# Kernel tuning notes

Hardware: AMD Instinct MI355X
Metric: run time of the kernel (lower is better)

Reference implementation:

```python
import jax, jax.numpy as jnp
import numpy as np

B = 2048
MAX_ATOMS = 32
ELEM = 83
LATENT = 64
LATTICE = 9


def _lin(k, fin, fout):
    k1, k2 = jax.random.split(k)
    s = 1.0 / np.sqrt(fin)
    return (jax.random.uniform(k1, (fin, fout), jnp.float32, -s, s),
            jax.random.uniform(k2, (fout,), jnp.float32, -s, s))


def setup_inputs() -> dict:
    key = jax.random.key(0)
    ks = jax.random.split(key, 32)
    inp = {}
    inp['elements'] = jax.random.randint(ks[0], (B, MAX_ATOMS), 0, ELEM)
    inp['coords'] = jax.random.uniform(ks[1], (B, MAX_ATOMS, 3), jnp.float32)
    inp['lattice'] = jax.random.normal(ks[2], (B, LATTICE), jnp.float32)
    inp['composition'] = jax.random.uniform(ks[3], (B, ELEM), jnp.float32)
    inp['eps'] = jax.random.normal(ks[4], (B, LATENT), jnp.float32)
    inp['emb_table'] = jax.random.normal(ks[5], (ELEM, 16), jnp.float32)
    inp['enc_w1'], inp['enc_b1'] = _lin(ks[6], 19, 256)
    inp['enc_w2'], inp['enc_b2'] = _lin(ks[7], 256, 128)
    inp['enc_w3'], inp['enc_b3'] = _lin(ks[8], 128, 128)
    inp['lat_w1'], inp['lat_b1'] = _lin(ks[9], LATTICE, 64)
    inp['lat_w2'], inp['lat_b2'] = _lin(ks[10], 64, 64)
    inp['mu_w'], inp['mu_b'] = _lin(ks[11], 192, LATENT)
    inp['lv_w'], inp['lv_b'] = _lin(ks[12], 192, LATENT)
    inp['dec_w1'], inp['dec_b1'] = _lin(ks[13], LATENT + ELEM, 512)
    s1 = 1.0 / np.sqrt(64 * 27)
    inp['ct1_w'] = jax.random.uniform(ks[14], (32, 64, 3, 3, 3), jnp.float32, -s1, s1)
    inp['ct1_b'] = jax.random.uniform(ks[15], (32,), jnp.float32, -s1, s1)
    s2 = 1.0 / np.sqrt(32 * 27)
    inp['ct2_w'] = jax.random.uniform(ks[16], (16, 32, 3, 3, 3), jnp.float32, -s2, s2)
    inp['ct2_b'] = jax.random.uniform(ks[17], (16,), jnp.float32, -s2, s2)
    inp['dec_w2'], inp['dec_b2'] = _lin(ks[18], 16 * 8 * 8 * 8, MAX_ATOMS * (ELEM + 3))
    inp['dl_w1'], inp['dl_b1'] = _lin(ks[19], LATENT, 64)
    inp['dl_w2'], inp['dl_b2'] = _lin(ks[20], 64, LATTICE)
    inp['gat1_w'], _ = _lin(ks[21], 19, 3 * 64)
    inp['gat1_b'] = jnp.zeros((3 * 64,), jnp.float32)
    inp['gat1_as'] = jax.random.normal(ks[22], (3, 64), jnp.float32) * 0.1
    inp['gat1_ad'] = jax.random.normal(ks[23], (3, 64), jnp.float32) * 0.1
    inp['gat2_w'], _ = _lin(ks[24], 192, 3)
    inp['gat2_b'] = jnp.zeros((3,), jnp.float32)
    inp['gat2_as'] = jax.random.normal(ks[25], (1, 3), jnp.float32) * 0.1
    inp['gat2_ad'] = jax.random.normal(ks[26], (1, 3), jnp.float32) * 0.1
    return inp


def _convT(x, w, b):
    # ConvTranspose3d(k=3, stride=2, pad=1, output_pad=1) == input-dilated conv
    y = jax.lax.conv_general_dilated(
        x, w, window_strides=(1, 1, 1),
        padding=((1, 2), (1, 2), (1, 2)), lhs_dilation=(2, 2, 2),
        dimension_numbers=('NCDHW', 'OIDHW', 'NCDHW'))
    return y + b[None, :, None, None, None]


def _gat(x, W, a_src, a_dst, bias, heads, out_ch, concat):
    # Dense (fully-connected per-sample graph) GATConv, eval mode (dropout off).
    Bn, N, F = x.shape
    h = jnp.einsum('bnf,fhc->bnhc', x, W.reshape(F, heads, out_ch))  # [B,N,H,C]
    s = jnp.einsum('bnhc,hc->bnh', h, a_src)  # source scores
    d = jnp.einsum('bnhc,hc->bnh', h, a_dst)  # target scores
    # e[b,i,j,h] for edge j->i (self-loops included in the full mesh)
    e = jax.nn.leaky_relu(d[:, :, None, :] + s[:, None, :, :], 0.2)
    a = jax.nn.softmax(e, axis=2)  # softmax over sources j per target i
    o = jnp.einsum('bijh,bjhc->bihc', a, h)
    if concat:
        return o.reshape(Bn, N, heads * out_ch) + bias
    return o.mean(axis=2) + bias


def reference(elements, coords, lattice, composition, eps, emb_table,
              enc_w1, enc_b1, enc_w2, enc_b2, enc_w3, enc_b3,
              lat_w1, lat_b1, lat_w2, lat_b2, mu_w, mu_b, lv_w, lv_b,
              dec_w1, dec_b1, ct1_w, ct1_b, ct2_w, ct2_b, dec_w2, dec_b2,
              dl_w1, dl_b1, dl_w2, dl_b2,
              gat1_w, gat1_b, gat1_as, gat1_ad,
              gat2_w, gat2_b, gat2_as, gat2_ad):
    Bn = coords.shape[0]
    # ---- encode ----
    af = jnp.concatenate([emb_table[elements], coords], axis=-1)  # [B,32,19]
    h = jax.nn.relu(af @ enc_w1 + enc_b1)
    h = jax.nn.relu(h @ enc_w2 + enc_b2)
    h = h @ enc_w3 + enc_b3
    g = h.mean(axis=1)  # [B,128]
    l = jax.nn.relu(lattice @ lat_w1 + lat_b1) @ lat_w2 + lat_b2
    comb = jnp.concatenate([g, l], axis=1)
    mu = comb @ mu_w + mu_b
    logvar = comb @ lv_w + lv_b
    z = mu + eps * jnp.exp(0.5 * logvar)
    # ---- decode ----
    d = jnp.concatenate([z, composition], axis=1) @ dec_w1 + dec_b1
    d = d.reshape(Bn, 64, 2, 2, 2)
    d = jax.nn.relu(_convT(d, ct1_w, ct1_b))   # [B,32,4,4,4]
    d = jax.nn.relu(_convT(d, ct2_w, ct2_b))   # [B,16,8,8,8]
    raw = (d.reshape(Bn, -1) @ dec_w2 + dec_b2).reshape(Bn, MAX_ATOMS, ELEM + 3)
    logits = raw[..., :ELEM]
    init_coords = jax.nn.sigmoid(raw[..., ELEM:])
    node = jnp.concatenate([emb_table[jnp.argmax(logits, axis=-1)], init_coords], axis=-1)  # [B,32,19]
    x = jax.nn.elu(_gat(node, gat1_w, gat1_as, gat1_ad, gat1_b, 3, 64, True))
    adj = jnp.tanh(_gat(x, gat2_w, gat2_as, gat2_ad, gat2_b, 1, 3, False)) * 0.1
    coords_out = jnp.mod(init_coords + adj, 1.0)
    recon = jnp.concatenate([logits, coords_out], axis=-1)  # [B,32,86]
    recon_lattice = jax.nn.relu(z @ dl_w1 + dl_b1) @ dl_w2 + dl_b2
    return (mu, logvar, recon, recon_lattice)
```

## Files before the change

kernel.cpp:

```cpp
#include <hip/hip_runtime.h>
#include <hip/hip_bf16.h>

typedef __hip_bfloat16 bf16;
typedef __attribute__((ext_vector_type(8))) __bf16 bf16x8;
typedef __attribute__((ext_vector_type(4))) float f32x4;

__device__ __forceinline__ float b2f(bf16 v){ return __bfloat162float(v); }
__device__ __forceinline__ bf16  f2b(float v){ return __float2bfloat16(v); }

template<typename T> __device__ __forceinline__ float ldf(const T* p, size_t i);
template<> __device__ __forceinline__ float ldf<float>(const float* p, size_t i){ return p[i]; }
template<> __device__ __forceinline__ float ldf<bf16 >(const bf16*  p, size_t i){ return b2f(p[i]); }

template<typename T> __device__ __forceinline__ void stf(T* p, size_t i, float v);
template<> __device__ __forceinline__ void stf<float>(float* p, size_t i, float v){ p[i] = v; }
template<> __device__ __forceinline__ void stf<bf16 >(bf16*  p, size_t i, float v){ p[i] = f2b(v); }

#define NATM 32
#define RECON_OFF 262144
#define RL_OFF    5898240

__device__ __forceinline__ void glds16(const bf16* g, bf16* l){
    __builtin_amdgcn_global_load_lds(
        (const __attribute__((address_space(1))) unsigned int*)g,
        (__attribute__((address_space(3))) unsigned int*)l,
        16, 0, 0);
}

__global__ __launch_bounds__(64) void k_detect(const void* emb, int* flag)
{
    __shared__ int cnt[64];
    const int t = threadIdx.x;
    const unsigned short* p = (const unsigned short*)emb;
    int c = 0;
    for (int i = t; i < 256; i += 64){
        int e = (p[i] >> 7) & 0xFF;
        c += (e >= 110 && e <= 132) ? 1 : 0;
    }
    cnt[t] = c;
    __syncthreads();
    if (t == 0){
        int s = 0;
        for (int i = 0; i < 64; i++) s += cnt[i];
        *flag = (s >= 200) ? 1 : 0;
    }
}

template<typename T>
__device__ __forceinline__ void prepEnc_impl(
    const T* w1, const T* b1, const T* w2, const T* b2,
    bf16* W1t, bf16* W2t, float* ebias)
{
    const int gt = blockIdx.x*256 + threadIdx.x;
    const int gs = gridDim.x*256;
    for (int e = gt; e < 8192; e += gs){
        int n = e >> 5, k = e & 31;
        W1t[e] = (k < 19) ? f2b(ldf(w1, (size_t)k*256 + n)) : f2b(0.f);
    }
    for (int e = gt; e < 32768; e += gs){
        int n = e >> 8, k = e & 255;
        W2t[e] = f2b(ldf(w2, (size_t)k*128 + n));
    }
    for (int i = gt; i < 384; i += gs)
        ebias[i] = (i < 256) ? ldf(b1, i) : ldf(b2, i-256);
}

__global__ __launch_bounds__(256) void k_prepEnc(
    const int* flag, const void* w1, const void* b1, const void* w2, const void* b2,
    bf16* W1t, bf16* W2t, float* ebias)
{
    if (*flag) prepEnc_impl<bf16>((const bf16*)w1,(const bf16*)b1,(const bf16*)w2,(const bf16*)b2, W1t, W2t, ebias);
    else       prepEnc_impl<float>((const float*)w1,(const float*)b1,(const float*)w2,(const float*)b2, W1t, W2t, ebias);
}

template<typename T>
__device__ __forceinline__ void buildA_impl(
    const int* elements, const T* coords, const T* emb, bf16* Abuf)
{
    const int r = blockIdx.x*256 + threadIdx.x;
    const int el = elements[r];
    bf16 row[32];
    #pragma unroll
    for (int f=0; f<16; f++) row[f] = f2b(ldf(emb, (size_t)el*16 + f));
    #pragma unroll
    for (int c=0; c<3; c++) row[16+c] = f2b(ldf(coords, (size_t)r*3 + c));
    #pragma unroll
    for (int f=19; f<32; f++) row[f] = f2b(0.f);
    *(int4*)(&Abuf[(size_t)r*32])      = *(int4*)(&row[0]);
    *(int4*)(&Abuf[(size_t)r*32 + 8])  = *(int4*)(&row[8]);
    *(int4*)(&Abuf[(size_t)r*32 + 16]) = *(int4*)(&row[16]);
    *(int4*)(&Abuf[(size_t)r*32 + 24]) = *(int4*)(&row[24]);
}

__global__ __launch_bounds__(256) void k_buildA(
    const int* flag, const int* elements, const void* coords, const void* emb, bf16* Abuf)
{
    if (*flag) buildA_impl<bf16>(elements,(const bf16*)coords,(const bf16*)emb, Abuf);
    else       buildA_impl<float>(elements,(const float*)coords,(const float*)emb, Abuf);
}

template<typename T>
__device__ __forceinline__ void pool_impl(
    const float* h2, const T* w3, const T* b3, float* gbuf)
{
    __shared__ float hsum[128];
    const int b = blockIdx.x, t = threadIdx.x;
    float s = 0.f;
    for (int n=0; n<32; n++) s += h2[(size_t)(b*32+n)*128 + t];
    hsum[t] = s;
    __syncthreads();
    float a = 0.f;
    for (int k=0; k<128; k++) a += hsum[k]*ldf(w3, (size_t)k*128 + t);
    gbuf[b*128+t] = a*(1.f/32.f) + ldf(b3, t);
}

__global__ __launch_bounds__(128) void k_pool(
    const int* flag, const float* h2, const void* w3, const void* b3, float* gbuf)
{
    if (*flag) pool_impl<bf16>(h2, (const bf16*)w3, (const bf16*)b3, gbuf);
    else       pool_impl<float>(h2, (const float*)w3, (const float*)b3, gbuf);
}

template<typename T>
__device__ __forceinline__ void enc_impl(
    const int* elements, const T* coords, const T* emb,
    const T* w1, const T* b1, const T* w2, const T* b2c,
    const T* w3, const T* b3, float* gbuf, char* smem)
{
    float (*af)[19]   = (float(*)[19])(smem);
    float (*h1)[256]  = (float(*)[256])(smem + 2432);
    float (*h2s)[128] = (float(*)[128])(smem + 35200);
    float* hsum       = (float*)(smem + 51584);
    const int b = blockIdx.x, t = threadIdx.x;

    for (int idx = t; idx < NATM*19; idx += 256){
        int n = idx/19, f = idx - n*19;
        af[n][f] = (f < 16) ? ldf(emb, (size_t)elements[b*NATM+n]*16 + f)
                            : ldf(coords, (size_t)(b*NATM+n)*3 + (f-16));
    }
    __syncthreads();
    {
        float wc[19];
        #pragma unroll
        for (int f=0; f<19; f++) wc[f] = ldf(w1, f*256 + t);
        float bb = ldf(b1, t);
        for (int n=0; n<NATM; n++){
            float a = bb;
            #pragma unroll
            for (int f=0; f<19; f++) a += af[n][f]*wc[f];
            h1[n][t] = fmaxf(a, 0.f);
        }
    }
    __syncthreads();
    {
        const int j = t & 127, half = t >> 7;
        float bb = ldf(b2c, j);
        float acc[16];
        #pragma unroll
        for (int n=0;n<16;n++) acc[n] = bb;
        for (int k=0;k<256;k+=4){
            float wa = ldf(w2, (k+0)*128+j);
            float wb = ldf(w2, (k+1)*128+j);
            float wcv= ldf(w2, (k+2)*128+j);
            float wd = ldf(w2, (k+3)*128+j);
            #pragma unroll
            for (int n=0;n<16;n++){
                float4 hv = *(const float4*)(&h1[half*16+n][k]);
                acc[n] += hv.x*wa + hv.y*wb + hv.z*wcv + hv.w*wd;
            }
        }
        #pragma unroll
        for (int n=0;n<16;n++) h2s[half*16+n][j] = fmaxf(acc[n], 0.f);
    }
    __syncthreads();
    if (t < 128){
        float s = 0.f;
        for (int n=0;n<NATM;n++) s += h2s[n][t];
        hsum[t] = s;
    }
    __syncthreads();
    if (t < 128){
        float a = 0.f;
        for (int k=0;k<128;k++) a += hsum[k]*ldf(w3, k*128+t);
        gbuf[b*128+t] = a*(1.f/32.f) + ldf(b3, t);
    }
}

__global__ __launch_bounds__(256) void k_encoder(
    const int* flag, const int* elements, const void* coords, const void* emb,
    const void* w1, const void* b1, const void* w2, const void* b2,
    const void* w3, const void* b3, float* gbuf)
{
    __shared__ __align__(16) char smem[52096];
    if (*flag) enc_impl<bf16>(elements,(const bf16*)coords,(const bf16*)emb,
        (const bf16*)w1,(const bf16*)b1,(const bf16*)w2,(const bf16*)b2,
        (const bf16*)w3,(const bf16*)b3, gbuf, smem);
    else       enc_impl<float>(elements,(const float*)coords,(const float*)emb,
        (const float*)w1,(const float*)b1,(const float*)w2,(const float*)b2,
        (const float*)w3,(const float*)b3, gbuf, smem);
}

template<typename T>
__device__ __forceinline__ void lat_impl(
    const T* lattice, const T* eps, const T* comp,
    const T* lw1, const T* lb1, const T* lw2, const T* lb2,
    const T* muw, const T* mub, const T* lvw, const T* lvb,
    const T* dw1, const T* db1, const T* dw2, const T* db2,
    const float* gbuf, float* zbuf, bf16* zc, void* d_out, char* smem)
{
    float* comb = (float*)(smem);
    float* lat  = (float*)(smem + 768);
    float* l1   = (float*)(smem + 832);
    float* zz   = (float*)(smem + 1088);
    float* r1   = (float*)(smem + 1344);
    T* out_mu = (T*)d_out;
    T* out_lv = out_mu + 131072;
    T* out_rl = out_mu + RL_OFF;
    const int b = blockIdx.x, t = threadIdx.x;
    comb[t]    = gbuf[b*128 + t];
    comb[64+t] = gbuf[b*128 + 64 + t];
    if (t < 9) lat[t] = ldf(lattice, b*9 + t);
    __syncthreads();
    {
        float a = ldf(lb1, t);
        #pragma unroll
        for (int f=0; f<9; f++) a += lat[f]*ldf(lw1, f*64+t);
        l1[t] = fmaxf(a, 0.f);
    }
    __syncthreads();
    {
        float a = ldf(lb2, t);
        for (int k=0;k<64;k++) a += l1[k]*ldf(lw2, k*64+t);
        comb[128+t] = a;
    }
    __syncthreads();
    float mu = ldf(mub, t), lv = ldf(lvb, t);
    for (int k=0;k<192;k++){
        float c = comb[k];
        mu += c*ldf(muw, k*64+t);
        lv += c*ldf(lvw, k*64+t);
    }
    float z = mu + ldf(eps, b*64+t)*expf(0.5f*lv);
    stf(out_mu, (size_t)b*64+t, mu);
    stf(out_lv, (size_t)b*64+t, lv);
    zbuf[b*64+t] = z;
    zz[t] = z;
    __syncthreads();
    if (zc){
        for (int i=t; i<160; i+=64){
            float v = (i<64) ? zz[i] : ((i<147) ? ldf(comp, b*83 + (i-64)) : 0.f);
            zc[(size_t)b*160 + i] = f2b(v);
        }
    }
    {
        float a = ldf(db1, t);
        for (int k=0;k<64;k++) a += zz[k]*ldf(dw1, k*64+t);
        r1[t] = fmaxf(a, 0.f);
    }
    __syncthreads();
    if (t < 9){
        float a = ldf(db2, t);
        for (int k=0;k<64;k++) a += r1[k]*ldf(dw2, k*9+t);
        stf(out_rl, (size_t)b*9+t, a);
    }
}

__global__ __launch_bounds__(64) void k_latent(
    const int* flag, const void* lattice, const void* eps, const void* comp,
    const void* lw1, const void* lb1, const void* lw2, const void* lb2,
    const void* muw, const void* mub, const void* lvw, const void* lvb,
    const void* dw1, const void* db1, const void* dw2, const void* db2,
    const float* gbuf, float* zbuf, bf16* zc, void* d_out)
{
    __shared__ __align__(16) char smem[1600];
    if (*flag) lat_impl<bf16>((const bf16*)lattice,(const bf16*)eps,(const bf16*)comp,
        (const bf16*)lw1,(const bf16*)lb1,(const bf16*)lw2,(const bf16*)lb2,
        (const bf16*)muw,(const bf16*)mub,(const bf16*)lvw,(const bf16*)lvb,
        (const bf16*)dw1,(const bf16*)db1,(const bf16*)dw2,(const bf16*)db2,
        gbuf, zbuf, zc, d_out, smem);
    else       lat_impl<float>((const float*)lattice,(const float*)eps,(const float*)comp,
        (const float*)lw1,(const float*)lb1,(const float*)lw2,(const float*)lb2,
        (const float*)muw,(const float*)mub,(const float*)lvw,(const float*)lvb,
        (const float*)dw1,(const float*)db1,(const float*)dw2,(const float*)db2,
        gbuf, zbuf, zc, d_out, smem);
}

template<typename T>
__device__ __forceinline__ void prep_impl(
    const T* db1, const T* c1b, const T* c2b, const T* db2, const T* dw1,
    float* biasf, bf16* BtW1)
{
    const int gt = blockIdx.x*256 + threadIdx.x;
    const int gs = gridDim.x*256;
    for (int i = gt; i < 3376; i += gs){
        float v;
        if (i < 512)      v = ldf(db1, i);
        else if (i < 544) v = ldf(c1b, i-512);
        else if (i < 560) v = ldf(c2b, i-544);
        else              v = (i-560 < 2752) ? ldf(db2, i-560) : 0.f;
        biasf[i] = v;
    }
    for (int e = gt; e < 512*160; e += gs){
        int n = e/160, k = e - n*160;
        BtW1[e] = f2b((k < 147) ? ldf(dw1, (size_t)k*512 + n) : 0.f);
    }
}

__global__ __launch_bounds__(256) void k_prep(
    const int* flag, const void* db1, const void* c1b, const void* c2b,
    const void* db2, const void* dw1, float* biasf, bf16* BtW1)
{
    if (*flag) prep_impl<bf16>((const bf16*)db1,(const bf16*)c1b,(const bf16*)c2b,
        (const bf16*)db2,(const bf16*)dw1, biasf, BtW1);
    else       prep_impl<float>((const float*)db1,(const float*)c1b,(const float*)c2b,
        (const float*)db2,(const float*)dw1, biasf, BtW1);
}

template<typename T>
__device__ __forceinline__ void expWc1_impl(const T* w, bf16* Wc1T)
{
    const int t = threadIdx.x;
    const int n = blockIdx.x*4 + (t >> 6);
    const int k0 = (t & 63) << 3;
    const int o = n >> 6, spo = n & 63;
    const int zd = spo >> 4, zh = (spo >> 2) & 3, zw = spo & 3;
    bf16 v8[8];
    #pragma unroll
    for (int j = 0; j < 8; j++){
        int k = k0 + j;
        int i = k >> 3, sp = k & 7;
        int td = sp >> 2, th = (sp >> 1) & 1, tw = sp & 1;
        int kd = 2*td + 1 - zd, kh = 2*th + 1 - zh, kw = 2*tw + 1 - zw;
        float v = 0.f;
        if (kd >= 0 && kd < 3 && kh >= 0 && kh < 3 && kw >= 0 && kw < 3)
            v = ldf(w, (size_t)(o*64 + i)*27 + kd*9 + kh*3 + kw);
        v8[j] = f2b(v);
    }
    *(int4*)(&Wc1T[(size_t)n*512 + k0]) = *(int4*)v8;
}

__global__ __launch_bounds__(256) void k_expWc1(const int* flag, const void* w, bf16* Wc1T)
{
    if (*flag) expWc1_impl<bf16>((const bf16*)w, Wc1T);
    else       expWc1_impl<float>((const float*)w, Wc1T);
}

template<typename T>
__device__ __forceinline__ void expWc2_impl(const T* w, bf16* Wc2T)
{
    const int n = blockIdx.x;
    const int k0 = threadIdx.x << 3;
    const int o = n >> 9, spo = n & 511;
    const int zd = spo >> 6, zh = (spo >> 3) & 7, zw = spo & 7;
    bf16 v8[8];
    #pragma unroll
    for (int j = 0; j < 8; j++){
        int k = k0 + j;
        int i = k >> 6, sp = k & 63;
        int td = sp >> 4, th = (sp >> 2) & 3, tw = sp & 3;
        int kd = 2*td + 1 - zd, kh = 2*th + 1 - zh, kw = 2*tw + 1 - zw;
        float v = 0.f;
        if (kd >= 0 && kd < 3 && kh >= 0 && kh < 3 && kw >= 0 && kw < 3)
            v = ldf(w, (size_t)(o*32 + i)*27 + kd*9 + kh*3 + kw);
        v8[j] = f2b(v);
    }
    *(int4*)(&Wc2T[(size_t)n*2048 + k0]) = *(int4*)v8;
}

__global__ __launch_bounds__(256) void k_expWc2(const int* flag, const void* w, bf16* Wc2T)
{
    if (*flag) expWc2_impl<bf16>((const bf16*)w, Wc2T);
    else       expWc2_impl<float>((const float*)w, Wc2T);
}

template<typename T>
__device__ __forceinline__ void transW_impl(const T* B, bf16* Bt)
{
    __shared__ bf16 tile[64][65];
    const int kb = blockIdx.x << 6;
    const int nb = blockIdx.y << 6;
    const int t = threadIdx.x;
    for (int idx=t; idx<4096; idx+=256){
        int k = idx>>6, n = idx&63;
        int col = nb + n;
        tile[k][n] = (col < 2752) ? f2b(ldf(B, (size_t)(kb+k)*2752 + col)) : f2b(0.f);
    }
    __syncthreads();
    for (int idx=t; idx<4096; idx+=256){
        int n = idx>>6, k = idx&63;
        Bt[(size_t)(nb+n)*8192 + kb + k] = tile[k][n];
    }
}

__global__ __launch_bounds__(256) void k_transW(const int* flag, const void* B, bf16* Bt)
{
    if (*flag) transW_impl<bf16>((const bf16*)B, Bt);
    else       transW_impl<float>((const float*)B, Bt);
}

struct GemmAcc { f32x4 a[4][4]; };

__device__ __forceinline__ void gemm128_core(
    const bf16* __restrict__ A, const bf16* __restrict__ Bt, int K,
    int bm, int bn, bf16* As, bf16* Bs, GemmAcc& G)
{
    const int t = threadIdx.x;
    const int w = t >> 6, lane = t & 63;
    const int wm = w >> 1, wn = w & 1;
    const int ml = lane & 15, mq = lane >> 4;
    const int lrow = lane >> 2;
    const int gchunk = (lane & 3) ^ ((lane >> 3) & 3);
    const int rchunk = (mq ^ ((ml >> 1) & 3)) << 3;

    const size_t arow = (size_t)(bm + w*32 + lrow);
    const size_t brow = (size_t)(bn + w*32 + lrow);

    for (int kt = 0; kt < K; kt += 32){
        __syncthreads();
        #pragma unroll
        for (int c = 0; c < 2; c++){
            glds16(A  + (arow + c*16)*K + kt + gchunk*8, &As[(w*32 + c*16)*32]);
            glds16(Bt + (brow + c*16)*K + kt + gchunk*8, &Bs[(w*32 + c*16)*32]);
        }
        __syncthreads();
        bf16x8 af[4], bfr[4];
        #pragma unroll
        for (int i=0;i<4;i++) af[i]  = *(const bf16x8*)(&As[(wm*64 + i*16 + ml)*32 + rchunk]);
        #pragma unroll
        for (int j=0;j<4;j++) bfr[j] = *(const bf16x8*)(&Bs[(wn*64 + j*16 + ml)*32 + rchunk]);
        #pragma unroll
        for (int i=0;i<4;i++)
            #pragma unroll
            for (int j=0;j<4;j++)
                G.a[i][j] = __builtin_amdgcn_mfma_f32_16x16x32_bf16(af[i], bfr[j], G.a[i][j], 0,0,0);
    }
}

template<typename OutT, int ACT>
__global__ __launch_bounds__(256) void k_gemm128(
    const bf16* __restrict__ A, const bf16* __restrict__ Bt, int K,
    const float* __restrict__ biasf, int bshift,
    OutT* __restrict__ C, int ldc)
{
    __shared__ __align__(16) bf16 As[128*32];
    __shared__ __align__(16) bf16 Bs[128*32];
    const int t = threadIdx.x;
    const int bm = blockIdx.x << 7, bn = blockIdx.y << 7;
    const int w = t >> 6, lane = t & 63;
    const int wm = w >> 1, wn = w & 1;
    const int ml = lane & 15, mq = lane >> 4;
    GemmAcc G;
    #pragma unroll
    for (int i=0;i<4;i++)
        #pragma unroll
        for (int j=0;j<4;j++) G.a[i][j] = (f32x4){0.f,0.f,0.f,0.f};
    gemm128_core(A, Bt, K, bm, bn, As, Bs, G);
    #pragma unroll
    for (int j=0;j<4;j++){
        const int col = bn + wn*64 + (j<<4) + ml;
        const float bv = biasf[col >> bshift];
        #pragma unroll
        for (int i=0;i<4;i++){
            #pragma unroll
            for (int r=0;r<4;r++){
                const int row = bm + wm*64 + (i<<4) + (mq<<2) + r;
                float v = G.a[i][j][r] + bv;
                if (ACT == 1) v = fmaxf(v, 0.f);
                stf(C, (size_t)row*ldc + col, v);
            }
        }
    }
}

__global__ __launch_bounds__(256) void k_gemm_recon64(
    const int* __restrict__ flag,
    const bf16* __restrict__ A, const bf16* __restrict__ Bt,
    const float* __restrict__ biasf, void* __restrict__ d_out)
{
    __shared__ __align__(16) bf16 As[64*32];
    __shared__ __align__(16) bf16 Bs[128*32];
    const int K = 8192;
    const int t = threadIdx.x;
    const int bm = blockIdx.x << 6, bn = blockIdx.y << 7;
    const int w = t >> 6, lane = t & 63;
    const int wm = w >> 1, wn = w & 1;
    const int ml = lane & 15, mq = lane >> 4;
    const int lrow = lane >> 2;
    const int gchunk = (lane & 3) ^ ((lane >> 3) & 3);
    const int rchunk = (mq ^ ((ml >> 1) & 3)) << 3;

    f32x4 acc[2][4];
    #pragma unroll
    for (int i=0;i<2;i++)
        #pragma unroll
        for (int j=0;j<4;j++) acc[i][j] = (f32x4){0.f,0.f,0.f,0.f};

    const size_t arow = (size_t)(bm + w*16 + lrow);
    const size_t brow = (size_t)(bn + w*32 + lrow);

    for (int kt = 0; kt < K; kt += 32){
        __syncthreads();
        glds16(A + arow*K + kt + gchunk*8, &As[(w*16)*32]);
        #pragma unroll
        for (int c = 0; c < 2; c++)
            glds16(Bt + (brow + c*16)*K + kt + gchunk*8, &Bs[(w*32 + c*16)*32]);
        __syncthreads();
        bf16x8 af[2], bfr[4];
        #pragma unroll
        for (int i=0;i<2;i++) af[i]  = *(const bf16x8*)(&As[(wm*32 + i*16 + ml)*32 + rchunk]);
        #pragma unroll
        for (int j=0;j<4;j++) bfr[j] = *(const bf16x8*)(&Bs[(wn*64 + j*16 + ml)*32 + rchunk]);
        #pragma unroll
        for (int i=0;i<2;i++)
            #pragma unroll
            for (int j=0;j<4;j++)
                acc[i][j] = __builtin_amdgcn_mfma_f32_16x16x32_bf16(af[i], bfr[j], acc[i][j], 0,0,0);
    }
    const int fl = *flag;
    #pragma unroll
    for (int j=0;j<4;j++){
        const int col = bn + wn*64 + (j<<4) + ml;
        if (col >= 2752) continue;
        const int f = col % 86;
        const float bv = biasf[560 + col];
        #pragma unroll
        for (int i=0;i<2;i++){
            #pragma unroll
            for (int r=0;r<4;r++){
                const int row = bm + wm*32 + (i<<4) + (mq<<2) + r;
                float v = acc[i][j][r] + bv;
                if (f >= 83) v = 1.f/(1.f + expf(-v));
                if (fl) stf((bf16*)d_out + RECON_OFF, (size_t)row*2752 + col, v);
                else    stf((float*)d_out + RECON_OFF, (size_t)row*2752 + col, v);
            }
        }
    }
}

template<typename T>
__device__ __forceinline__ void conv_impl(
    const float* zbuf, const T* comp,
    const T* dw1, const T* db1, const T* c1w, const T* c1b,
    const T* c2w, const T* c2b, bf16* Amat, char* smem)
{
    float* zc        = (float*)(smem);
    float (*d0s)[8]  = (float(*)[8])(smem + 640);
    float (*c1s)[64] = (float(*)[64])(smem + 2688);
    bf16* w2s        = (bf16*)(smem + 10880);
    const int b = blockIdx.x, t = threadIdx.x;
    for (int i=t; i<16*32*27; i+=256) w2s[i] = f2b(ldf(c2w, i));
    if (t < 147) zc[t] = (t < 64) ? zbuf[b*64+t] : ldf(comp, b*83 + (t-64));
    __syncthreads();
    #pragma unroll
    for (int jj=0; jj<2; jj++){
        int j = t + (jj<<8);
        float a = ldf(db1, j);
        for (int k=0;k<147;k++) a += zc[k]*ldf(dw1, k*512+j);
        d0s[j>>3][j&7] = a;
    }
    __syncthreads();
    {
        const int o = t>>3;
        const float bias = ldf(c1b, o);
        const T* wb = c1w + o*64*27;
        for (int u=0; u<8; u++){
            int sp = (t&7) + (u<<3);
            int zd = sp>>4, zh = (sp>>2)&3, zw = sp&3;
            float acc = bias;
            for (int kd=0;kd<3;kd++){
                int qd = zd+kd-1; if (qd<0 || (qd&1) || qd>=4) continue; int td=qd>>1;
                for (int kh=0;kh<3;kh++){
                    int qh = zh+kh-1; if (qh<0 || (qh&1) || qh>=4) continue; int th=qh>>1;
                    for (int kw=0;kw<3;kw++){
                        int qw = zw+kw-1; if (qw<0 || (qw&1) || qw>=4) continue; int tw=qw>>1;
                        const int koff = kd*9+kh*3+kw;
                        const int spi = td*4+th*2+tw;
                        float s = 0.f;
                        #pragma unroll 8
                        for (int i=0;i<64;i++) s += ldf(wb, i*27+koff)*d0s[i][spi];
                        acc += s;
                    }
                }
            }
            c1s[o][sp] = fmaxf(acc, 0.f);
        }
    }
    __syncthreads();
    {
        const int o = t>>4;
        const float bias = ldf(c2b, o);
        for (int u=0; u<32; u++){
            int sp = (t&15) + (u<<4);
            int zd = sp>>6, zh=(sp>>3)&7, zw=sp&7;
            float acc = bias;
            for (int kd=0;kd<3;kd++){
                int qd = zd+kd-1; if (qd<0 || (qd&1) || qd>=8) continue; int td=qd>>1;
                for (int kh=0;kh<3;kh++){
                    int qh = zh+kh-1; if (qh<0 || (qh&1) || qh>=8) continue; int th=qh>>1;
                    for (int kw=0;kw<3;kw++){
                        int qw = zw+kw-1; if (qw<0 || (qw&1) || qw>=8) continue; int tw=qw>>1;
                        const int koff = kd*9+kh*3+kw;
                        const int spi = td*16+th*4+tw;
                        const int wbase = (o*32)*27 + koff;
                        float s = 0.f;
                        #pragma unroll 8
                        for (int i=0;i<32;i++) s += b2f(w2s[wbase + i*27])*c1s[i][spi];
                        acc += s;
                    }
                }
            }
            Amat[(size_t)b*8192 + o*512 + sp] = f2b(fmaxf(acc, 0.f));
        }
    }
}

__global__ __launch_bounds__(256) void k_conv(
    const int* flag, const float* zbuf, const void* comp,
    const void* dw1, const void* db1, const void* c1w, const void* c1b,
    const void* c2w, const void* c2b, bf16* Amat)
{
    __shared__ __align__(16) char smem[38528];
    if (*flag) conv_impl<bf16>(zbuf,(const bf16*)comp,(const bf16*)dw1,(const bf16*)db1,
        (const bf16*)c1w,(const bf16*)c1b,(const bf16*)c2w,(const bf16*)c2b, Amat, smem);
    else       conv_impl<float>(zbuf,(const float*)comp,(const float*)dw1,(const float*)db1,
        (const float*)c1w,(const float*)c1b,(const float*)c2w,(const float*)c2b, Amat, smem);
}

template<typename T> struct BStage;
template<> struct BStage<bf16>{
    static __device__ __forceinline__ void go(const bf16* p, bf16* v8){
        union{ int4 q; bf16 e[8]; } u; u.q = *(const int4*)p;
        #pragma unroll
        for (int j=0;j<8;j++) v8[j] = u.e[j];
    }
};
template<> struct BStage<float>{
    static __device__ __forceinline__ void go(const float* p, bf16* v8){
        float4 a = *(const float4*)p, b = *(const float4*)(p+4);
        v8[0]=f2b(a.x); v8[1]=f2b(a.y); v8[2]=f2b(a.z); v8[3]=f2b(a.w);
        v8[4]=f2b(b.x); v8[5]=f2b(b.y); v8[6]=f2b(b.z); v8[7]=f2b(b.w);
    }
};

__device__ __forceinline__ bf16x8 readBfrag(const bf16 (*Bs)[42], int n, int k0){
    union { bf16x8 v; unsigned int u[4]; } r;
    const unsigned int* p = (const unsigned int*)(&Bs[n][k0]);
    r.u[0]=p[0]; r.u[1]=p[1]; r.u[2]=p[2]; r.u[3]=p[3];
    return r.v;
}

template<typename T>
__device__ __forceinline__ void gemm_impl(
    const bf16* A, const T* B, const T* bias, void* d_out, char* smem)
{
    bf16 (*As)[40] = (bf16(*)[40])(smem);
    bf16 (*Bs)[42] = (bf16(*)[42])(smem + 10240);
    T* out_recon = (T*)d_out + RECON_OFF;
    const int t = threadIdx.x;
    const int bm = blockIdx.x << 7;
    const int bn = blockIdx.y << 6;
    const int w = t >> 6, lane = t & 63;
    const int ml = lane & 15, mq = lane >> 4;
    f32x4 acc[2][4];
    #pragma unroll
    for (int i=0;i<2;i++)
        #pragma unroll
        for (int j=0;j<4;j++) acc[i][j] = (f32x4){0.f,0.f,0.f,0.f};

    const int sm = t >> 2;
    const int sk = (t & 3) << 3;
    const int kk = t >> 3;
    const int nn = (t & 7) << 3;

    for (int kt = 0; kt < 8192; kt += 32){
        __syncthreads();
        {
            int4 v0 = *(const int4*)(A + (size_t)(bm + sm     )*8192 + kt + sk);
            int4 v1 = *(const int4*)(A + (size_t)(bm + sm + 64)*8192 + kt + sk);
            *(int4*)(&As[sm][sk])    = v0;
            *(int4*)(&As[sm+64][sk]) = v1;
            bf16 bv[8];
            BStage<T>::go(B + (size_t)(kt + kk)*2752 + bn + nn, bv);
            #pragma unroll
            for (int j=0;j<8;j++) Bs[nn+j][kk] = bv[j];
        }
        __syncthreads();
        bf16x8 a0 = *(const bf16x8*)(&As[(w<<5) + ml     ][mq<<3]);
        bf16x8 a1 = *(const bf16x8*)(&As[(w<<5) + 16 + ml][mq<<3]);
        bf16x8 b0 = readBfrag(Bs, ml,      mq<<3);
        bf16x8 b1 = readBfrag(Bs, 16 + ml, mq<<3);
        bf16x8 b2 = readBfrag(Bs, 32 + ml, mq<<3);
        bf16x8 b3 = readBfrag(Bs, 48 + ml, mq<<3);
        acc[0][0] = __builtin_amdgcn_mfma_f32_16x16x32_bf16(a0,b0,acc[0][0],0,0,0);
        acc[0][1] = __builtin_amdgcn_mfma_f32_16x16x32_bf16(a0,b1,acc[0][1],0,0,0);
        acc[0][2] = __builtin_amdgcn_mfma_f32_16x16x32_bf16(a0,b2,acc[0][2],0,0,0);
        acc[0][3] = __builtin_amdgcn_mfma_f32_16x16x32_bf16(a0,b3,acc[0][3],0,0,0);
        acc[1][0] = __builtin_amdgcn_mfma_f32_16x16x32_bf16(a1,b0,acc[1][0],0,0,0);
        acc[1][1] = __builtin_amdgcn_mfma_f32_16x16x32_bf16(a1,b1,acc[1][1],0,0,0);
        acc[1][2] = __builtin_amdgcn_mfma_f32_16x16x32_bf16(a1,b2,acc[1][2],0,0,0);
        acc[1][3] = __builtin_amdgcn_mfma_f32_16x16x32_bf16(a1,b3,acc[1][3],0,0,0);
    }
    #pragma unroll
    for (int nt=0; nt<4; nt++){
        const int col = bn + (nt<<4) + ml;
        const int atom = col / 86;
        const int f = col - atom*86;
        const float bv = ldf(bias, col);
        #pragma unroll
        for (int mt=0; mt<2; mt++){
            #pragma unroll
            for (int r=0; r<4; r++){
                const int row = bm + (w<<5) + (mt<<4) + (mq<<2) + r;
                float v = acc[mt][nt][r] + bv;
                if (f >= 83) v = 1.f/(1.f + expf(-v));
                stf(out_recon, (size_t)row*2752 + col, v);
            }
        }
    }
}

__global__ __launch_bounds__(256) void k_gemm(
    const int* flag, const bf16* A, const void* B, const void* bias, void* d_out)
{
    __shared__ __align__(16) char smem[15616];
    if (*flag) gemm_impl<bf16>(A, (const bf16*)B, (const bf16*)bias, d_out, smem);
    else       gemm_impl<float>(A, (const float*)B, (const float*)bias, d_out, smem);
}

template<typename T>
__device__ __forceinline__ void gat_impl(
    const T* emb, const T* g1w, const T* g1b, const T* g1as, const T* g1ad,
    const T* g2w, const T* g2b, const T* g2as, const T* g2ad,
    void* d_out, char* smem)
{
    float* ic    = (float*)(smem);
    int*   amaxs = (int*)  (smem + 384);
    float* hs    = (float*)(smem + 512);
    float* xs    = (float*)(smem + 25088);
    float* U     = (float*)(smem + 49664);
    float* sa    = (float*)(smem + 61952);
    float* da    = (float*)(smem + 62336);
    float* hh    = (float*)(smem + 62720);
    float* s2    = (float*)(smem + 63104);
    float* d2    = (float*)(smem + 63232);
    float* lg    = xs;
    float* node  = U;
    float* att   = U;
    float* att2  = U;

    T* out_recon = (T*)d_out + RECON_OFF;
    const int b = blockIdx.x, t = threadIdx.x;

    for (int i=t; i<2656; i+=256){
        int n = i/83, f = i - n*83;
        lg[i] = ldf(out_recon, (size_t)b*2752 + n*86 + f);
    }
    if (t < 96){
        int n = t/3, c = t - 3*(t/3);
        ic[t] = ldf(out_recon, (size_t)b*2752 + n*86 + 83 + c);
    }
    __syncthreads();
    if (t < 32){
        const float* lp = lg + t*83;
        float best = lp[0]; int bi = 0;
        for (int f=1; f<83; f++){ float v = lp[f]; if (v > best){ best=v; bi=f; } }
        amaxs[t] = bi;
    }
    __syncthreads();
    for (int i=t; i<608; i+=256){
        int n = i/19, f = i - n*19;
        node[n*19+f] = (f<16) ? ldf(emb, amaxs[n]*16+f) : ic[n*3 + (f-16)];
    }
    __syncthreads();
    if (t < 192){
        float wc[19];
        #pragma unroll
        for (int f=0;f<19;f++) wc[f] = ldf(g1w, f*192+t);
        for (int n=0;n<32;n++){
            float a = 0.f;
            #pragma unroll
            for (int f=0;f<19;f++) a += node[n*19+f]*wc[f];
            hs[n*192+t] = a;
        }
    }
    __syncthreads();
    if (t < 96){
        int n = t/3, hd = t - 3*(t/3);
        float s=0.f, d=0.f;
        for (int c=0;c<64;c++){
            float hv = hs[n*192 + hd*64 + c];
            s += hv*ldf(g1as, hd*64+c);
            d += hv*ldf(g1ad, hd*64+c);
        }
        sa[n*3+hd] = s; da[n*3+hd] = d;
    }
    __syncthreads();
    if (t < 96){
        int i = t/3, hd = t - 3*(t/3);
        float di = da[i*3+hd];
        float ev[32]; float m = -1e30f;
        for (int j=0;j<32;j++){
            float e = di + sa[j*3+hd];
            e = (e > 0.f) ? e : 0.2f*e;
            ev[j] = e; m = fmaxf(m, e);
        }
        float ssum = 0.f;
        for (int j=0;j<32;j++){ float p = expf(ev[j]-m); ev[j]=p; ssum += p; }
        float inv = 1.f/ssum;
        for (int j=0;j<32;j++) att[(i*3+hd)*32 + j] = ev[j]*inv;
    }
    __syncthreads();
    if (t < 192){
        const int hd = t >> 6;
        float bb = ldf(g1b, t);
        float a[32];
        #pragma unroll
        for (int i=0;i<32;i++) a[i] = 0.f;
        for (int j=0;j<32;j++){
            float hv = hs[j*192+t];
            #pragma unroll
            for (int i=0;i<32;i++) a[i] += att[(i*3+hd)*32 + j]*hv;
        }
        for (int i=0;i<32;i++){
            float v = a[i] + bb;
            xs[i*192+t] = (v > 0.f) ? v : (expf(v) - 1.f);
        }
    }
    __syncthreads();
    if (t < 96){
        int n = t/3, c = t - 3*(t/3);
        float a = 0.f;
        for (int f=0;f<192;f++) a += xs[n*192+f]*ldf(g2w, f*3+c);
        hh[n*3+c] = a;
    }
    __syncthreads();
    if (t < 32){
        float s=0.f,d=0.f;
        #pragma unroll
        for (int c=0;c<3;c++){ s += hh[t*3+c]*ldf(g2as,c); d += hh[t*3+c]*ldf(g2ad,c); }
        s2[t]=s; d2[t]=d;
    }
    __syncthreads();
    if (t < 32){
        float di = d2[t];
        float ev[32]; float m=-1e30f;
        for (int j=0;j<32;j++){
            float e = di + s2[j]; e = (e>0.f)?e:0.2f*e; ev[j]=e; m=fmaxf(m,e);
        }
        float ssum=0.f;
        for (int j=0;j<32;j++){ float p=expf(ev[j]-m); ev[j]=p; ssum+=p; }
        float inv = 1.f/ssum;
        for (int j=0;j<32;j++) att2[t*32+j] = ev[j]*inv;
    }
    __syncthreads();
    if (t < 96){
        int i = t/3, c = t - 3*(t/3);
        float a = 0.f;
        for (int j=0;j<32;j++) a += att2[i*32+j]*hh[j*3+c];
        a += ldf(g2b, c);
        float adj = tanhf(a)*0.1f;
        float cr = ic[i*3+c] + adj;
        cr -= floorf(cr);
        stf(out_recon, (size_t)b*2752 + i*86 + 83 + c, cr);
    }
}

__global__ __launch_bounds__(256) void k_gat(
    const int* flag, const void* emb,
    const void* g1w, const void* g1b, const void* g1as, const void* g1ad,
    const void* g2w, const void* g2b, const void* g2as, const void* g2ad,
    void* d_out)
{
    __shared__ __align__(16) char smem[63360];
    if (*flag) gat_impl<bf16>((const bf16*)emb,(const bf16*)g1w,(const bf16*)g1b,
        (const bf16*)g1as,(const bf16*)g1ad,(const bf16*)g2w,(const bf16*)g2b,
        (const bf16*)g2as,(const bf16*)g2ad, d_out, smem);
    else       gat_impl<float>((const float*)emb,(const float*)g1w,(const float*)g1b,
        (const float*)g1as,(const float*)g1ad,(const float*)g2w,(const float*)g2b,
        (const float*)g2as,(const float*)g2ad, d_out, smem);
}

extern "C" void kernel_launch(void* const* d_in, const int* in_sizes, int n_in,
                              void* d_out, int out_size, void* d_ws, size_t ws_size,
                              hipStream_t stream)
{
    (void)in_sizes; (void)n_in; (void)out_size;
    char* ws = (char*)d_ws;
    const bool big = (ws_size >= 83000000ull);

    if (big){
        bf16*  Abuf  = (bf16*)(ws);
        bf16*  h1    = (bf16*)(ws + 4194304);
        float* h2    = (float*)(ws + 37748736);
        bf16*  Amat  = (bf16*)(ws);
        bf16*  Wc2T  = (bf16*)(ws + 33554432);
        bf16*  BtW2  = (bf16*)(ws + 33554432);
        bf16*  c1    = (bf16*)(ws + 67108864);
        bf16*  d0    = (bf16*)(ws + 75497472);
        bf16*  Wc1T  = (bf16*)(ws + 77594624);
        bf16*  zc    = (bf16*)(ws + 79691776);
        bf16*  BtW1  = (bf16*)(ws + 80347136);
        float* biasf = (float*)(ws + 80510976);
        float* gbuf  = (float*)(ws + 80524480);
        float* zbuf  = (float*)(ws + 81573056);
        int*   flag  = (int*)  (ws + 82097344);
        bf16*  W1t   = (bf16*)(ws + 82097408);
        bf16*  W2t   = (bf16*)(ws + 82113792);
        float* ebias = (float*)(ws + 82179328);

        k_detect<<<1, 64, 0, stream>>>(d_in[5], flag);
        k_prepEnc<<<64, 256, 0, stream>>>(flag, d_in[6], d_in[7], d_in[8], d_in[9], W1t, W2t, ebias);
        k_buildA<<<256, 256, 0, stream>>>(flag, (const int*)d_in[0], d_in[1], d_in[5], Abuf);
        k_gemm128<bf16,1> <<<dim3(512,2), 256, 0, stream>>>(Abuf, W1t, 32,  ebias,     0, h1, 256);
        k_gemm128<float,1><<<dim3(512,1), 256, 0, stream>>>(h1,   W2t, 256, ebias+256, 0, h2, 128);
        k_pool<<<2048, 128, 0, stream>>>(flag, h2, d_in[10], d_in[11], gbuf);
        k_latent<<<2048, 64, 0, stream>>>(flag, d_in[2], d_in[4], d_in[3],
            d_in[12], d_in[13], d_in[14], d_in[15],
            d_in[16], d_in[17], d_in[18], d_in[19],
            d_in[28], d_in[29], d_in[30], d_in[31],
            gbuf, zbuf, zc, d_out);
        k_prep<<<64, 256, 0, stream>>>(flag, d_in[21], d_in[23], d_in[25], d_in[27], d_in[20], biasf, BtW1);
        k_expWc1<<<512, 256, 0, stream>>>(flag, d_in[22], Wc1T);
        k_expWc2<<<8192, 256, 0, stream>>>(flag, d_in[24], Wc2T);
        k_gemm128<bf16,0><<<dim3(16,4),  256, 0, stream>>>(zc, BtW1, 160,  biasf,     0, d0,   512);
        k_gemm128<bf16,1><<<dim3(16,16), 256, 0, stream>>>(d0, Wc1T, 512,  biasf+512, 6, c1,   2048);
        k_gemm128<bf16,1><<<dim3(16,64), 256, 0, stream>>>(c1, Wc2T, 2048, biasf+544, 9, Amat, 8192);
        k_transW<<<dim3(128,44), 256, 0, stream>>>(flag, d_in[26], BtW2);
        k_gemm_recon64<<<dim3(32,22), 256, 0, stream>>>(flag, Amat, BtW2, biasf, d_out);
        k_gat<<<2048, 256, 0, stream>>>(flag, d_in[5],
            d_in[32], d_in[33], d_in[34], d_in[35],
            d_in[36], d_in[37], d_in[38], d_in[39], d_out);
    } else {
        bf16*  Amat = (bf16*)(ws);
        float* gbuf = (float*)(ws + 33554432);
        float* zbuf = (float*)(ws + 34603008);
        int*   flag = (int*)  (ws + 35127296);

        k_detect<<<1, 64, 0, stream>>>(d_in[5], flag);
        k_encoder<<<2048, 256, 0, stream>>>(flag, (const int*)d_in[0], d_in[1], d_in[5],
            d_in[6], d_in[7], d_in[8], d_in[9], d_in[10], d_in[11], gbuf);
        k_latent<<<2048, 64, 0, stream>>>(flag, d_in[2], d_in[4], d_in[3],
            d_in[12], d_in[13], d_in[14], d_in[15],
            d_in[16], d_in[17], d_in[18], d_in[19],
            d_in[28], d_in[29], d_in[30], d_in[31],
            gbuf, zbuf, (bf16*)nullptr, d_out);
        k_conv<<<2048, 256, 0, stream>>>(flag, zbuf, d_in[3],
            d_in[20], d_in[21], d_in[22], d_in[23], d_in[24], d_in[25], Amat);
        k_gemm<<<dim3(16,43), 256, 0, stream>>>(flag, Amat, d_in[26], d_in[27], d_out);
        k_gat<<<2048, 256, 0, stream>>>(flag, d_in[5],
            d_in[32], d_in[33], d_in[34], d_in[35],
            d_in[36], d_in[37], d_in[38], d_in[39], d_out);
    }
}
```

Baseline: 708.0 us.

## Use 64-deep K tiles for bf16 GEMMs and merge weight-prep kernels

Adds a GEMM core that stages 64-wide K slices per iteration with an XOR swizzle and applies it to the encoder second layer, both transposed-conv GEMMs and the recon GEMM. This halves the number of barrier-separated load/compute rounds and doubles the MFMA work done per shared-memory stage, at the cost of more LDS per block and possibly lower occupancy. It also folds three weight-preparation kernels (encoder, decoder bias/W1, conv1 expansion) into one launch with a larger grid to cut launch overhead.

New measurement: 639.0 us. -9.7%, faster.

```diff
diff --git a/kernel.cpp b/kernel.cpp
--- a/kernel.cpp
+++ b/kernel.cpp
@@ -47,9 +47,11 @@
 }
 
 template<typename T>
-__device__ __forceinline__ void prepEnc_impl(
+__device__ __forceinline__ void prepAll_impl(
     const T* w1, const T* b1, const T* w2, const T* b2,
-    bf16* W1t, bf16* W2t, float* ebias)
+    const T* db1, const T* c1b, const T* c2b, const T* db2, const T* dw1,
+    const T* c1w,
+    bf16* W1t, bf16* W2t, float* ebias, float* biasf, bf16* BtW1, bf16* Wc1T)
 {
     const int gt = blockIdx.x*256 + threadIdx.x;
     const int gs = gridDim.x*256;
@@ -63,14 +65,52 @@
     }
     for (int i = gt; i < 384; i += gs)
         ebias[i] = (i < 256) ? ldf(b1, i) : ldf(b2, i-256);
-}
-
-__global__ __launch_bounds__(256) void k_prepEnc(
-    const int* flag, const void* w1, const void* b1, const void* w2, const void* b2,
-    bf16* W1t, bf16* W2t, float* ebias)
-{
-    if (*flag) prepEnc_impl<bf16>((const bf16*)w1,(const bf16*)b1,(const bf16*)w2,(const bf16*)b2, W1t, W2t, ebias);
-    else       prepEnc_impl<float>((const float*)w1,(const float*)b1,(const float*)w2,(const float*)b2, W1t, W2t, ebias);
+    for (int i = gt; i < 3376; i += gs){
+        float v;
+        if (i < 512)      v = ldf(db1, i);
+        else if (i < 544) v = ldf(c1b, i-512);
+        else if (i < 560) v = ldf(c2b, i-544);
+        else              v = (i-560 < 2752) ? ldf(db2, i-560) : 0.f;
+        biasf[i] = v;
+    }
+    for (int e = gt; e < 512*160; e += gs){
+        int n = e/160, k = e - n*160;
+        BtW1[e] = f2b((k < 147) ? ldf(dw1, (size_t)k*512 + n) : 0.f);
+    }
+    for (int g = gt; g < 2048*64; g += gs){
+        const int n = g >> 6;
+        const int k0 = (g & 63) << 3;
+        const int o = n >> 6, spo = n & 63;
+        const int zd = spo >> 4, zh = (spo >> 2) & 3, zw = spo & 3;
+        bf16 v8[8];
+        #pragma unroll
+        for (int j = 0; j < 8; j++){
+            int k = k0 + j;
+            int i = k >> 3, sp = k & 7;
+            int td = sp >> 2, th = (sp >> 1) & 1, tw = sp & 1;
+            int kd = 2*td + 1 - zd, kh = 2*th + 1 - zh, kw = 2*tw + 1 - zw;
+            float v = 0.f;
+            if (kd >= 0 && kd < 3 && kh >= 0 && kh < 3 && kw >= 0 && kw < 3)
+                v = ldf(c1w, (size_t)(o*64 + i)*27 + kd*9 + kh*3 + kw);
+            v8[j] = f2b(v);
+        }
+        *(int4*)(&Wc1T[(size_t)n*512 + k0]) = *(int4*)v8;
+    }
+}
+
+__global__ __launch_bounds__(256) void k_prepAll(
+    const int* flag,
+    const void* w1, const void* b1, const void* w2, const void* b2,
+    const void* db1, const void* c1b, const void* c2b, const void* db2, const void* dw1,
+    const void* c1w,
+    bf16* W1t, bf16* W2t, float* ebias, float* biasf, bf16* BtW1, bf16* Wc1T)
+{
+    if (*flag) prepAll_impl<bf16>((const bf16*)w1,(const bf16*)b1,(const bf16*)w2,(const bf16*)b2,
+        (const bf16*)db1,(const bf16*)c1b,(const bf16*)c2b,(const bf16*)db2,(const bf16*)dw1,
+        (const bf16*)c1w, W1t, W2t, ebias, biasf, BtW1, Wc1T);
+    else       prepAll_impl<float>((const float*)w1,(const float*)b1,(const float*)w2,(const float*)b2,
+        (const float*)db1,(const float*)c1b,(const float*)c2b,(const float*)db2,(const float*)dw1,
+        (const float*)c1w, W1t, W2t, ebias, biasf, BtW1, Wc1T);
 }
 
 template<typename T>
@@ -286,66 +326,6 @@
 }
 
 template<typename T>
-__device__ __forceinline__ void prep_impl(
-    const T* db1, const T* c1b, const T* c2b, const T* db2, const T* dw1,
-    float* biasf, bf16* BtW1)
-{
-    const int gt = blockIdx.x*256 + threadIdx.x;
-    const int gs = gridDim.x*256;
-    for (int i = gt; i < 3376; i += gs){
-        float v;
-        if (i < 512)      v = ldf(db1, i);
-        else if (i < 544) v = ldf(c1b, i-512);
-        else if (i < 560) v = ldf(c2b, i-544);
-        else              v = (i-560 < 2752) ? ldf(db2, i-560) : 0.f;
-        biasf[i] = v;
-    }
-    for (int e = gt; e < 512*160; e += gs){
-        int n = e/160, k = e - n*160;
-        BtW1[e] = f2b((k < 147) ? ldf(dw1, (size_t)k*512 + n) : 0.f);
-    }
-}
-
-__global__ __launch_bounds__(256) void k_prep(
-    const int* flag, const void* db1, const void* c1b, const void* c2b,
-    const void* db2, const void* dw1, float* biasf, bf16* BtW1)
-{
-    if (*flag) prep_impl<bf16>((const bf16*)db1,(const bf16*)c1b,(const bf16*)c2b,
-        (const bf16*)db2,(const bf16*)dw1, biasf, BtW1);
-    else       prep_impl<float>((const float*)db1,(const float*)c1b,(const float*)c2b,
-        (const float*)db2,(const float*)dw1, biasf, BtW1);
-}
-
-template<typename T>
-__device__ __forceinline__ void expWc1_impl(const T* w, bf16* Wc1T)
-{
-    const int t = threadIdx.x;
-    const int n = blockIdx.x*4 + (t >> 6);
-    const int k0 = (t & 63) << 3;
-    const int o = n >> 6, spo = n & 63;
-    const int zd = spo >> 4, zh = (spo >> 2) & 3, zw = spo & 3;
-    bf16 v8[8];
-    #pragma unroll
-    for (int j = 0; j < 8; j++){
-        int k = k0 + j;
-        int i = k >> 3, sp = k & 7;
-        int td = sp >> 2, th = (sp >> 1) & 1, tw = sp & 1;
-        int kd = 2*td + 1 - zd, kh = 2*th + 1 - zh, kw = 2*tw + 1 - zw;
-        float v = 0.f;
-        if (kd >= 0 && kd < 3 && kh >= 0 && kh < 3 && kw >= 0 && kw < 3)
-            v = ldf(w, (size_t)(o*64 + i)*27 + kd*9 + kh*3 + kw);
-        v8[j] = f2b(v);
-    }
-    *(int4*)(&Wc1T[(size_t)n*512 + k0]) = *(int4*)v8;
-}
-
-__global__ __launch_bounds__(256) void k_expWc1(const int* flag, const void* w, bf16* Wc1T)
-{
-    if (*flag) expWc1_impl<bf16>((const bf16*)w, Wc1T);
-    else       expWc1_impl<float>((const float*)w, Wc1T);
-}
-
-template<typename T>
 __device__ __forceinline__ void expWc2_impl(const T* w, bf16* Wc2T)
 {
     const int n = blockIdx.x;
@@ -472,50 +452,110 @@
     }
 }
 
-__global__ __launch_bounds__(256) void k_gemm_recon64(
+template<int BM>
+__device__ __forceinline__ void gemm64_core(
+    const bf16* __restrict__ A, const bf16* __restrict__ Bt, int K,
+    int bm, int bn, bf16* As, bf16* Bs, f32x4 acc[][4])
+{
+    const int t = threadIdx.x;
+    const int w = t >> 6, lane = t & 63;
+    const int wm = w >> 1, wn = w & 1;
+    const int ml = lane & 15, mq = lane >> 4;
+    const int lrow = lane >> 3;
+    const int gch  = (lane & 7) ^ lrow;
+    const int mswz = ml & 7;
+
+    const size_t abase = (size_t)(bm + w*(BM/4) + lrow);
+    const size_t bbase = (size_t)(bn + w*32 + lrow);
+
+    for (int kt = 0; kt < K; kt += 64){
+        __syncthreads();
+        #pragma unroll
+        for (int c = 0; c < BM/32; c++)
+            glds16(A + (abase + c*8)*K + kt + gch*8, &As[(w*(BM/4) + c*8)*64]);
+        #pragma unroll
+        for (int c = 0; c < 4; c++)
+            glds16(Bt + (bbase + c*8)*K + kt + gch*8, &Bs[(w*32 + c*8)*64]);
+        __syncthreads();
+        bf16x8 af[2][BM/32], bfr[2][4];
+        #pragma unroll
+        for (int ks=0; ks<2; ks++){
+            #pragma unroll
+            for (int i=0;i<BM/32;i++){
+                const int r = wm*(BM/2) + i*16 + ml;
+                af[ks][i] = *(const bf16x8*)(&As[r*64 + (((ks<<2)+mq) ^ mswz)*8]);
+            }
+            #pragma unroll
+            for (int j=0;j<4;j++){
+                const int r = wn*64 + j*16 + ml;
+                bfr[ks][j] = *(const bf16x8*)(&Bs[r*64 + (((ks<<2)+mq) ^ mswz)*8]);
+            }
+        }
+        #pragma unroll
+        for (int ks=0; ks<2; ks++)
+            #pragma unroll
+            for (int i=0;i<BM/32;i++)
+                #pragma unroll
+                for (int j=0;j<4;j++)
+                    acc[i][j] = __builtin_amdgcn_mfma_f32_16x16x32_bf16(af[ks][i], bfr[ks][j], acc[i][j], 0,0,0);
+    }
+}
+
+template<typename OutT, int ACT>
+__global__ __launch_bounds__(256) void k_gemm64(
+    const bf16* __restrict__ A, const bf16* __restrict__ Bt, int K,
+    const float* __restrict__ biasf, int bshift,
+    OutT* __restrict__ C, int ldc)
+{
+    __shared__ __align__(16) bf16 As[128*64];
+    __shared__ __align__(16) bf16 Bs[128*64];
+    const int t = threadIdx.x;
+    const int bm = blockIdx.x << 7, bn = blockIdx.y << 7;
+    const int w = t >> 6, lane = t & 63;
+    const int wm = w >> 1, wn = w & 1;
+    const int ml = lane & 15, mq = lane >> 4;
+    f32x4 acc[4][4];
+    #pragma unroll
+    for (int i=0;i<4;i++)
+        #pragma unroll
+        for (int j=0;j<4;j++) acc[i][j] = (f32x4){0.f,0.f,0.f,0.f};
+    gemm64_core<128>(A, Bt, K, bm, bn, As, Bs, acc);
+    #pragma unroll
+    for (int j=0;j<4;j++){
+        const int col = bn + wn*64 + (j<<4) + ml;
+        const float bv = biasf[col >> bshift];
+        #pragma unroll
+        for (int i=0;i<4;i++){
+            #pragma unroll
+            for (int r=0;r<4;r++){
+                const int row = bm + wm*64 + (i<<4) + (mq<<2) + r;
+                float v = acc[i][j][r] + bv;
+                if (ACT == 1) v = fmaxf(v, 0.f);
+                stf(C, (size_t)row*ldc + col, v);
+            }
+        }
+    }
+}
+
+__global__ __launch_bounds__(256) void k_gemm64_recon(
     const int* __restrict__ flag,
     const bf16* __restrict__ A, const bf16* __restrict__ Bt,
     const float* __restrict__ biasf, void* __restrict__ d_out)
 {
-    __shared__ __align__(16) bf16 As[64*32];
-    __shared__ __align__(16) bf16 Bs[128*32];
+    __shared__ __align__(16) bf16 As[64*64];
+    __shared__ __align__(16) bf16 Bs[128*64];
     const int K = 8192;
     const int t = threadIdx.x;
     const int bm = blockIdx.x << 6, bn = blockIdx.y << 7;
     const int w = t >> 6, lane = t & 63;
     const int wm = w >> 1, wn = w & 1;
     const int ml = lane & 15, mq = lane >> 4;
-    const int lrow = lane >> 2;
-    const int gchunk = (lane & 3) ^ ((lane >> 3) & 3);
-    const int rchunk = (mq ^ ((ml >> 1) & 3)) << 3;
-
     f32x4 acc[2][4];
     #pragma unroll
     for (int i=0;i<2;i++)
         #pragma unroll
         for (int j=0;j<4;j++) acc[i][j] = (f32x4){0.f,0.f,0.f,0.f};
-
-    const size_t arow = (size_t)(bm + w*16 + lrow);
-    const size_t brow = (size_t)(bn + w*32 + lrow);
-
-    for (int kt = 0; kt < K; kt += 32){
-        __syncthreads();
-        glds16(A + arow*K + kt + gchunk*8, &As[(w*16)*32]);
-        #pragma unroll
-        for (int c = 0; c < 2; c++)
-            glds16(Bt + (brow + c*16)*K + kt + gchunk*8, &Bs[(w*32 + c*16)*32]);
-        __syncthreads();
-        bf16x8 af[2], bfr[4];
-        #pragma unroll
-        for (int i=0;i<2;i++) af[i]  = *(const bf16x8*)(&As[(wm*32 + i*16 + ml)*32 + rchunk]);
-        #pragma unroll
-        for (int j=0;j<4;j++) bfr[j] = *(const bf16x8*)(&Bs[(wn*64 + j*16 + ml)*32 + rchunk]);
-        #pragma unroll
-        for (int i=0;i<2;i++)
-            #pragma unroll
-            for (int j=0;j<4;j++)
-                acc[i][j] = __builtin_amdgcn_mfma_f32_16x16x32_bf16(af[i], bfr[j], acc[i][j], 0,0,0);
-    }
+    gemm64_core<64>(A, Bt, K, bm, bn, As, Bs, acc);
     const int fl = *flag;
     #pragma unroll
     for (int j=0;j<4;j++){
@@ -909,24 +949,26 @@
         float* ebias = (float*)(ws + 82179328);
 
         k_detect<<<1, 64, 0, stream>>>(d_in[5], flag);
-        k_prepEnc<<<64, 256, 0, stream>>>(flag, d_in[6], d_in[7], d_in[8], d_in[9], W1t, W2t, ebias);
+        k_prepAll<<<512, 256, 0, stream>>>(flag,
+            d_in[6], d_in[7], d_in[8], d_in[9],
+            d_in[21], d_in[23], d_in[25], d_in[27], d_in[20],
+            d_in[22],
+            W1t, W2t, ebias, biasf, BtW1, Wc1T);
         k_buildA<<<256, 256, 0, stream>>>(flag, (const int*)d_in[0], d_in[1], d_in[5], Abuf);
-        k_gemm128<bf16,1> <<<dim3(512,2), 256, 0, stream>>>(Abuf, W1t, 32,  ebias,     0, h1, 256);
-        k_gemm128<float,1><<<dim3(512,1), 256, 0, stream>>>(h1,   W2t, 256, ebias+256, 0, h2, 128);
+        k_gemm128<bf16,1><<<dim3(512,2), 256, 0, stream>>>(Abuf, W1t, 32,  ebias,     0, h1, 256);
+        k_gemm64<float,1><<<dim3(512,1), 256, 0, stream>>>(h1,   W2t, 256, ebias+256, 0, h2, 128);
         k_pool<<<2048, 128, 0, stream>>>(flag, h2, d_in[10], d_in[11], gbuf);
         k_latent<<<2048, 64, 0, stream>>>(flag, d_in[2], d_in[4], d_in[3],
             d_in[12], d_in[13], d_in[14], d_in[15],
             d_in[16], d_in[17], d_in[18], d_in[19],
             d_in[28], d_in[29], d_in[30], d_in[31],
             gbuf, zbuf, zc, d_out);
-        k_prep<<<64, 256, 0, stream>>>(flag, d_in[21], d_in[23], d_in[25], d_in[27], d_in[20], biasf, BtW1);
-        k_expWc1<<<512, 256, 0, stream>>>(flag, d_in[22], Wc1T);
         k_expWc2<<<8192, 256, 0, stream>>>(flag, d_in[24], Wc2T);
         k_gemm128<bf16,0><<<dim3(16,4),  256, 0, stream>>>(zc, BtW1, 160,  biasf,     0, d0,   512);
-        k_gemm128<bf16,1><<<dim3(16,16), 256, 0, stream>>>(d0, Wc1T, 512,  biasf+512, 6, c1,   2048);
-        k_gemm128<bf16,1><<<dim3(16,64), 256, 0, stream>>>(c1, Wc2T, 2048, biasf+544, 9, Amat, 8192);
+        k_gemm64<bf16,1><<<dim3(16,16),  256, 0, stream>>>(d0, Wc1T, 512,  biasf+512, 6, c1,   2048);
+        k_gemm64<bf16,1><<<dim3(16,64),  256, 0, stream>>>(c1, Wc2T, 2048, biasf+544, 9, Amat, 8192);
         k_transW<<<dim3(128,44), 256, 0, stream>>>(flag, d_in[26], BtW2);
-        k_gemm_recon64<<<dim3(32,22), 256, 0, stream>>>(flag, Amat, BtW2, biasf, d_out);
+        k_gemm64_recon<<<dim3(32,22), 256, 0, stream>>>(flag, Amat, BtW2, biasf, d_out);
         k_gat<<<2048, 256, 0, stream>>>(flag, d_in[5],
             d_in[32], d_in[33], d_in[34], d_in[35],
             d_in[36], d_in[37], d_in[38], d_in[39], d_out);
```
